# Optimization experiments

Hardware: AMD Instinct MI355X
Metric: run time of the kernel (lower is better)

Reference implementation:

```python
import math
import jax, jax.numpy as jnp
import numpy as np

C, B, T, D = 8, 4, 8192, 64
MAX_LEN = 8192
_DELTA = math.log2(MAX_LEN) / max(C - 1, 1)
# lam_c = 1 - 2^{-(c*delta)}; lam_0 == 0 (memoryless channel)
LAMBDAS = jnp.array([1.0 - 2.0 ** (-(c * _DELTA)) for c in range(C)], dtype=jnp.float32)


def setup_inputs() -> dict:
    key = jax.random.key(0)
    k0, k1, k2 = jax.random.split(key, 3)
    return {
        "channels": jax.random.normal(k0, (C, B, T, D), dtype=jnp.float32),
        "gw_fwd": jax.random.normal(k1, (C, D, D), dtype=jnp.float32) * 0.02,
        "gb_fwd": jnp.ones((C, D), dtype=jnp.float32),
        "gw_bwd": jax.random.normal(k2, (C, D, D), dtype=jnp.float32) * 0.02,
        "gb_bwd": jnp.ones((C, D), dtype=jnp.float32),
    }


def _fixed_decay_scan(lam, v):
    """h_t = lam * h_{t-1} + v_t over axis=1 (time); v: [B,T,D], lam scalar.
    For lam==0 this reduces to identity, matching the torch fast path."""
    a = jnp.full_like(v, lam)

    def combine(x, y):
        a1, b1 = x
        a2, b2 = y
        return (a1 * a2, a2 * b1 + b2)

    return jax.lax.associative_scan(combine, (a, v), axis=1)[1]


def _run_direction(channels, W, b):
    # torch Linear: y = x @ W.T + b, W is (out,in) -> einsum 'cbtd,ced->cbte'
    g = jax.nn.sigmoid(jnp.einsum('cbtd,ced->cbte', channels, W) + b[:, None, None, :])
    gated = g * channels
    return jax.vmap(_fixed_decay_scan)(LAMBDAS, gated)  # [C,B,T,D]


def reference(channels, gw_fwd, gb_fwd, gw_bwd, gb_bwd):
    fwd = _run_direction(channels, gw_fwd, gb_fwd)
    rev = channels[:, :, ::-1, :]
    bwd = _run_direction(rev, gw_bwd, gb_bwd)[:, :, ::-1, :]
    return fwd, bwd
```

## Files before the change

### kernel.cpp

```cpp
#include <hip/hip_runtime.h>
#include <cmath>
#include <cstdint>

typedef __attribute__((ext_vector_type(8))) short short8;
typedef __attribute__((ext_vector_type(4))) float f32x4;
typedef __attribute__((ext_vector_type(2))) unsigned int u32x2;

struct Lams { float v[8]; };

#define NC 8
#define NB 4
#define NT 8192
#define ND 64
#define CL 128
#define NK (NT / CL)
#define NSLOT (2 * NC * NB * NK)
#define LDH 72

__device__ __forceinline__ uint32_t pk2(float lo, float hi) {
    uint32_t r;
    asm("v_cvt_pk_bf16_f32 %0, %1, %2" : "=v"(r) : "v"(lo), "v"(hi));
    return r;
}

__device__ __forceinline__ float bf2f(unsigned short s) {
    return __builtin_bit_cast(float, (uint32_t)s << 16);
}

__global__ __launch_bounds__(256, 6) void k1_fused(
    const float* __restrict__ x, const float* __restrict__ Wf,
    const float* __restrict__ bf, const float* __restrict__ Wb,
    const float* __restrict__ bb, float* __restrict__ out,
    int* __restrict__ flags, float* __restrict__ evals, Lams lams)
{
    __shared__ unsigned short xbuf[CL * LDH];
    __shared__ float ends_lds[4][ND];
    __shared__ float hprev_lds[ND];

    const int tid  = threadIdx.x;
    const int lane = tid & 63;
    const int w    = tid >> 6;

    int idx = blockIdx.x;
    const int k   = idx & (NK - 1); idx >>= 6;
    const int b   = idx & (NB - 1); idx >>= 2;
    const int c   = idx & (NC - 1); idx >>= 3;
    const int dir = idx;

    const float lam = lams.v[c];
    const float* W    = (dir ? Wb : Wf) + c * ND * ND;
    const float* bias = (dir ? bb : bf) + c * ND;
    const float* xb   = x + (size_t)(c * NB + b) * NT * ND;
    float* ob = out + (size_t)dir * (size_t)(NC*NB*NT*ND)
                    + (size_t)(c * NB + b) * NT * ND;

    const int er = lane & 15;
    const int ks = lane >> 4;

    const int tr0 = k * CL;
    const int r0  = w * 32;

    {
        const int sr = lane >> 4;
        const int sc = (lane & 15) * 4;
        if (dir == 0) {
            const float* p = xb + (size_t)(tr0 + r0 + sr) * ND + sc;
            #pragma unroll
            for (int g = 0; g < 8; ++g) {
                f32x4 v = *reinterpret_cast<const f32x4*>(p + (size_t)g * 4 * ND);
                u32x2 q = { pk2(v[0], v[1]), pk2(v[2], v[3]) };
                *reinterpret_cast<u32x2*>(&xbuf[(r0 + g*4 + sr) * LDH + sc]) = q;
            }
        } else {
            const float* p = xb + (size_t)(NT-1 - (tr0 + r0 + sr)) * ND + sc;
            #pragma unroll
            for (int g = 0; g < 8; ++g) {
                f32x4 v = *reinterpret_cast<const f32x4*>(p - (size_t)g * 4 * ND);
                u32x2 q = { pk2(v[0], v[1]), pk2(v[2], v[3]) };
                *reinterpret_cast<u32x2*>(&xbuf[(r0 + g*4 + sr) * LDH + sc]) = q;
            }
        }
    }

    short8 bfrag[4][2];
    #pragma unroll
    for (int et = 0; et < 4; ++et) {
        const float* wr = W + (et*16 + er) * ND + ks * 8;
        #pragma unroll
        for (int kk = 0; kk < 2; ++kk) {
            f32x4 lo = *reinterpret_cast<const f32x4*>(wr + kk*32);
            f32x4 hi = *reinterpret_cast<const f32x4*>(wr + kk*32 + 4);
            union { short8 s8; uint32_t u[4]; } t;
            t.u[0] = pk2(lo[0], lo[1]); t.u[1] = pk2(lo[2], lo[3]);
            t.u[2] = pk2(hi[0], hi[1]); t.u[3] = pk2(hi[2], hi[3]);
            bfrag[et][kk] = t.s8;
        }
    }
    float bias_r[4];
    #pragma unroll
    for (int et = 0; et < 4; ++et) bias_r[et] = bias[et*16 + er];

    #pragma unroll
    for (int u = 0; u < 2; ++u) {
        const int rl0 = r0 + u*16;
        short8 afrag[2];
        afrag[0] = *reinterpret_cast<const short8*>(&xbuf[(rl0 + er) * LDH + ks * 8]);
        afrag[1] = *reinterpret_cast<const short8*>(&xbuf[(rl0 + er) * LDH + 32 + ks * 8]);
        #pragma unroll
        for (int et = 0; et < 4; ++et) {
            f32x4 acc = {0.f, 0.f, 0.f, 0.f};
            acc = __builtin_amdgcn_mfma_f32_16x16x32_bf16(afrag[0], bfrag[et][0], acc, 0,0,0);
            acc = __builtin_amdgcn_mfma_f32_16x16x32_bf16(afrag[1], bfrag[et][1], acc, 0,0,0);
            const int col = et*16 + er;
            float gated[4];
            #pragma unroll
            for (int r = 0; r < 4; ++r) {
                const int rl = rl0 + ks*4 + r;
                float z  = acc[r] + bias_r[et];
                float g  = __builtin_amdgcn_rcpf(1.0f + __expf(-z));
                float xv = bf2f(xbuf[rl * LDH + col]);
                gated[r] = g * xv;
            }
            uint32_t p01 = pk2(gated[0], gated[1]);
            uint32_t p23 = pk2(gated[2], gated[3]);
            xbuf[(rl0 + ks*4 + 0) * LDH + col] = (unsigned short)(p01 & 0xFFFF);
            xbuf[(rl0 + ks*4 + 1) * LDH + col] = (unsigned short)(p01 >> 16);
            xbuf[(rl0 + ks*4 + 2) * LDH + col] = (unsigned short)(p23 & 0xFFFF);
            xbuf[(rl0 + ks*4 + 3) * LDH + col] = (unsigned short)(p23 >> 16);
        }
    }

    float lam32 = lam*lam; lam32*=lam32; lam32*=lam32; lam32*=lam32; lam32*=lam32;

    {
        float h = 0.f;
        #pragma unroll
        for (int i = 0; i < 32; ++i) {
            const int a = (r0 + i) * LDH + lane;
            float v = bf2f(xbuf[a]);
            h = fmaf(h, lam, v);
            xbuf[a] = (unsigned short)(pk2(h, h) & 0xFFFF);
        }
        ends_lds[w][lane] = h;
    }
    __syncthreads();

    const int slot = blockIdx.x;
    if (w == 3) {
        float carry3 = 0.f;
        #pragma unroll
        for (int j = 0; j < 3; ++j) carry3 = fmaf(carry3, lam32, ends_lds[j][lane]);
        float E = fmaf(carry3, lam32, ends_lds[3][lane]);

        float Hprev = 0.f;
        if (c != 0) {
            __hip_atomic_store(&evals[(size_t)slot * ND + lane], E,
                               __ATOMIC_RELAXED, __HIP_MEMORY_SCOPE_AGENT);
            asm volatile("s_waitcnt vmcnt(0)" ::: "memory");
            if (lane == 0)
                __hip_atomic_store(&flags[slot], 1, __ATOMIC_RELAXED,
                                   __HIP_MEMORY_SCOPE_AGENT);
            if (k != 0) {
                const int base = slot - k;
                if (lane < k) {
                    while (__hip_atomic_load(&flags[base + lane], __ATOMIC_RELAXED,
                                             __HIP_MEMORY_SCOPE_AGENT) == 0)
                        __builtin_amdgcn_s_sleep(8);
                }
                asm volatile("" ::: "memory");
                const float* eb = evals + (size_t)base * ND;
                float l1 = lam32 * lam32; l1 *= l1;
                float l4 = l1 * l1; l4 *= l4;
                float P = 0.f;
                int j = 0;
                const int rem = k & 3;
                for (; j < rem; ++j)
                    P = fmaf(P, l1, eb[(size_t)j * ND + lane]);
                for (; j < k; j += 4) {
                    float e0 = eb[(size_t)(j+0) * ND + lane];
                    float e1 = eb[(size_t)(j+1) * ND + lane];
                    float e2 = eb[(size_t)(j+2) * ND + lane];
                    float e3 = eb[(size_t)(j+3) * ND + lane];
                    float t = fmaf(fmaf(fmaf(e0, l1, e1), l1, e2), l1, e3);
                    P = fmaf(P, l4, t);
                }
                Hprev = P;
            }
        }
        hprev_lds[lane] = Hprev;
    }
    __syncthreads();

    float carry = 0.f, pw = 1.f;
    for (int j = 0; j < w; ++j) {
        carry = fmaf(carry, lam32, ends_lds[j][lane]);
        pw *= lam32;
    }
    carry = fmaf(pw, hprev_lds[lane], carry);

    float f = lam;
    if (dir == 0) {
        float* p = ob + (size_t)(tr0 + r0) * ND + lane;
        #pragma unroll
        for (int i = 0; i < 32; ++i) {
            float h = bf2f(xbuf[(r0 + i) * LDH + lane]);
            p[(size_t)i * ND] = fmaf(f, carry, h);
            f *= lam;
        }
    } else {
        float* p = ob + (size_t)(NT-1 - (tr0 + r0)) * ND + lane;
        #pragma unroll
        for (int i = 0; i < 32; ++i) {
            float h = bf2f(xbuf[(r0 + i) * LDH + lane]);
            *(p - (size_t)i * ND) = fmaf(f, carry, h);
            f *= lam;
        }
    }
}

extern "C" void kernel_launch(void* const* d_in, const int* in_sizes, int n_in,
                              void* d_out, int out_size, void* d_ws, size_t ws_size,
                              hipStream_t stream)
{
    const float* x  = (const float*)d_in[0];
    const float* Wf = (const float*)d_in[1];
    const float* bf = (const float*)d_in[2];
    const float* Wb = (const float*)d_in[3];
    const float* bb = (const float*)d_in[4];
    float* out = (float*)d_out;

    int*   flags = (int*)d_ws;
    float* evals = (float*)((char*)d_ws + NSLOT * 4);

    Lams lams;
    const double delta = 13.0 / 7.0;
    for (int c = 0; c < 8; ++c)
        lams.v[c] = (float)(1.0 - pow(2.0, -(double)c * delta));

    hipMemsetAsync(flags, 0, NSLOT * 4, stream);

    dim3 grid(NSLOT);
    k1_fused<<<grid, 256, 0, stream>>>(x, Wf, bf, Wb, bb, out, flags, evals, lams);
}
```

Baseline: 83.82 us.

## Double chunk length to 256 rows with 8 waves and vectorize output stores

Each block now handles 256 time steps with 512 threads (8 waves). This halves the number of chunks and shortens the cross-block decoupled-lookback chain and its flag polling. The final output write is reorganised so each lane stores four contiguous floats via float4, with per-column carries, instead of per-lane scalar stores. Larger LDS use per block (about 36 KB) may reduce occupancy, and the serial carry prefix across waves is longer.

```diff
diff --git a/kernel.cpp b/kernel.cpp
--- a/kernel.cpp
+++ b/kernel.cpp
@@ -12,9 +12,10 @@
 #define NB 4
 #define NT 8192
 #define ND 64
-#define CL 128
+#define CL 256
 #define NK (NT / CL)
 #define NSLOT (2 * NC * NB * NK)
+#define NWAVE 8
 #define LDH 72
 
 __device__ __forceinline__ uint32_t pk2(float lo, float hi) {
@@ -27,14 +28,14 @@
     return __builtin_bit_cast(float, (uint32_t)s << 16);
 }
 
-__global__ __launch_bounds__(256, 6) void k1_fused(
+__global__ __launch_bounds__(512, 8) void k1_fused(
     const float* __restrict__ x, const float* __restrict__ Wf,
     const float* __restrict__ bf, const float* __restrict__ Wb,
     const float* __restrict__ bb, float* __restrict__ out,
     int* __restrict__ flags, float* __restrict__ evals, Lams lams)
 {
     __shared__ unsigned short xbuf[CL * LDH];
-    __shared__ float ends_lds[4][ND];
+    __shared__ float ends_lds[NWAVE][ND];
     __shared__ float hprev_lds[ND];
 
     const int tid  = threadIdx.x;
@@ -42,7 +43,7 @@
     const int w    = tid >> 6;
 
     int idx = blockIdx.x;
-    const int k   = idx & (NK - 1); idx >>= 6;
+    const int k   = idx & (NK - 1); idx >>= 5;
     const int b   = idx & (NB - 1); idx >>= 2;
     const int c   = idx & (NC - 1); idx >>= 3;
     const int dir = idx;
@@ -146,11 +147,12 @@
     __syncthreads();
 
     const int slot = blockIdx.x;
-    if (w == 3) {
-        float carry3 = 0.f;
-        #pragma unroll
-        for (int j = 0; j < 3; ++j) carry3 = fmaf(carry3, lam32, ends_lds[j][lane]);
-        float E = fmaf(carry3, lam32, ends_lds[3][lane]);
+    if (w == NWAVE - 1) {
+        float carryW = 0.f;
+        #pragma unroll
+        for (int j = 0; j < NWAVE - 1; ++j)
+            carryW = fmaf(carryW, lam32, ends_lds[j][lane]);
+        float E = fmaf(carryW, lam32, ends_lds[NWAVE-1][lane]);
 
         float Hprev = 0.f;
         if (c != 0) {
@@ -169,7 +171,7 @@
                 }
                 asm volatile("" ::: "memory");
                 const float* eb = evals + (size_t)base * ND;
-                float l1 = lam32 * lam32; l1 *= l1;
+                float l1 = lam32*lam32; l1 *= l1; l1 *= l1;
                 float l4 = l1 * l1; l4 *= l4;
                 float P = 0.f;
                 int j = 0;
@@ -191,29 +193,51 @@
     }
     __syncthreads();
 
-    float carry = 0.f, pw = 1.f;
-    for (int j = 0; j < w; ++j) {
-        carry = fmaf(carry, lam32, ends_lds[j][lane]);
-        pw *= lam32;
-    }
-    carry = fmaf(pw, hprev_lds[lane], carry);
-
-    float f = lam;
-    if (dir == 0) {
-        float* p = ob + (size_t)(tr0 + r0) * ND + lane;
-        #pragma unroll
-        for (int i = 0; i < 32; ++i) {
-            float h = bf2f(xbuf[(r0 + i) * LDH + lane]);
-            p[(size_t)i * ND] = fmaf(f, carry, h);
-            f *= lam;
-        }
-    } else {
-        float* p = ob + (size_t)(NT-1 - (tr0 + r0)) * ND + lane;
-        #pragma unroll
-        for (int i = 0; i < 32; ++i) {
-            float h = bf2f(xbuf[(r0 + i) * LDH + lane]);
-            *(p - (size_t)i * ND) = fmaf(f, carry, h);
-            f *= lam;
+    {
+        const int sr = lane >> 4;
+        const int dg = lane & 15;
+        float carry4[4];
+        #pragma unroll
+        for (int j2 = 0; j2 < 4; ++j2) {
+            const int d = dg*4 + j2;
+            float cy = 0.f, pw = 1.f;
+            for (int j = 0; j < w; ++j) {
+                cy = fmaf(cy, lam32, ends_lds[j][d]);
+                pw *= lam32;
+            }
+            carry4[j2] = fmaf(pw, hprev_lds[d], cy);
+        }
+        const float lam2 = lam * lam, lam4 = lam2 * lam2;
+        float f = lam;
+        for (int j = 0; j < sr; ++j) f *= lam;
+        if (dir == 0) {
+            float* p = ob + (size_t)(tr0 + r0 + sr) * ND + dg*4;
+            #pragma unroll
+            for (int g = 0; g < 8; ++g) {
+                u32x2 hv = *reinterpret_cast<const u32x2*>(
+                    &xbuf[(r0 + g*4 + sr) * LDH + dg*4]);
+                f32x4 o;
+                o[0] = fmaf(f, carry4[0], bf2f((unsigned short)(hv[0] & 0xFFFF)));
+                o[1] = fmaf(f, carry4[1], bf2f((unsigned short)(hv[0] >> 16)));
+                o[2] = fmaf(f, carry4[2], bf2f((unsigned short)(hv[1] & 0xFFFF)));
+                o[3] = fmaf(f, carry4[3], bf2f((unsigned short)(hv[1] >> 16)));
+                *reinterpret_cast<f32x4*>(p + (size_t)g * 4 * ND) = o;
+                f *= lam4;
+            }
+        } else {
+            float* p = ob + (size_t)(NT-1 - (tr0 + r0 + sr)) * ND + dg*4;
+            #pragma unroll
+            for (int g = 0; g < 8; ++g) {
+                u32x2 hv = *reinterpret_cast<const u32x2*>(
+                    &xbuf[(r0 + g*4 + sr) * LDH + dg*4]);
+                f32x4 o;
+                o[0] = fmaf(f, carry4[0], bf2f((unsigned short)(hv[0] & 0xFFFF)));
+                o[1] = fmaf(f, carry4[1], bf2f((unsigned short)(hv[0] >> 16)));
+                o[2] = fmaf(f, carry4[2], bf2f((unsigned short)(hv[1] & 0xFFFF)));
+                o[3] = fmaf(f, carry4[3], bf2f((unsigned short)(hv[1] >> 16)));
+                *reinterpret_cast<f32x4*>(p - (size_t)g * 4 * ND) = o;
+                f *= lam4;
+            }
         }
     }
 }
@@ -230,7 +254,7 @@
     float* out = (float*)d_out;
 
     int*   flags = (int*)d_ws;
-    float* evals = (float*)((char*)d_ws + NSLOT * 4);
+    float* evals = (float*)((char*)d_ws + 16384);
 
     Lams lams;
     const double delta = 13.0 / 7.0;
@@ -240,5 +264,5 @@
     hipMemsetAsync(flags, 0, NSLOT * 4, stream);
 
     dim3 grid(NSLOT);
-    k1_fused<<<grid, 256, 0, stream>>>(x, Wf, bf, Wb, bb, out, flags, evals, lams);
-}
+    k1_fused<<<grid, 512, 0, stream>>>(x, Wf, bf, Wb, bb, out, flags, evals, lams);
+}
```

After: 80.90 us. -3.5%, faster.
